# Optimization experiments

Hardware: AMD Instinct MI355X
Metric: run time of the kernel (lower is better)

The kernel has to match this reference:

```python
import jax, jax.numpy as jnp
import numpy as np

LN_EPS = 1e-5

def layernorm(x, w, b):
    mu = jnp.mean(x, axis=-1, keepdims=True)
    var = jnp.mean(jnp.square(x - mu), axis=-1, keepdims=True)
    return (x - mu) * jax.lax.rsqrt(var + LN_EPS) * w + b

def l2_normalize(x, eps=1e-12):
    n = jnp.sqrt(jnp.sum(jnp.square(x), axis=-1, keepdims=True))
    return x / jnp.maximum(n, eps)

def setup_inputs() -> dict:
    key = jax.random.key(0)
    k1, k2 = jax.random.split(key)
    B, D, Npix = 8, 64, 32768
    K, P = 19, 5
    return {
        "base_feature": jax.random.normal(k1, (B, D, Npix), dtype=jnp.float32),
        "means": jax.random.normal(k2, (K, P, D), dtype=jnp.float32) * 0.02,  # trunc_normal_(std=0.02)
        "diagonal": jnp.ones((K, P, D), dtype=jnp.float32),
        "feat_w": jnp.ones((D,), dtype=jnp.float32),
        "feat_b": jnp.zeros((D,), dtype=jnp.float32),
        "mask_w": jnp.ones((K,), dtype=jnp.float32),
        "mask_b": jnp.zeros((K,), dtype=jnp.float32),
    }

def gmm_log_prob(x, mu, scale):
    # x: [N, D]; mu, scale: [KP, D]  (MultivariateNormalDiag with scale_diag=scale)
    # log p = -0.5 * sum(((x-mu)/s)^2) - sum(log s) - 0.5*D*log(2*pi)
    D = x.shape[-1]
    inv2 = 1.0 / jnp.square(scale)                      # [KP, D]
    quad = (jnp.square(x) @ inv2.T                       # [N, KP]
            - 2.0 * (x @ (mu * inv2).T)
            + jnp.sum(jnp.square(mu) * inv2, axis=-1))
    log_norm = jnp.sum(jnp.log(scale), axis=-1) + 0.5 * D * jnp.log(2.0 * jnp.pi)
    return -0.5 * quad - log_norm                        # [N, KP]

def reference(base_feature, means, diagonal, feat_w, feat_b, mask_w, mask_b):
    B, D, Npix = base_feature.shape
    K, P, _ = means.shape
    # 'b c n -> (b n) c'
    _c = jnp.transpose(base_feature, (0, 2, 1)).reshape(B * Npix, D)
    _c = layernorm(_c, feat_w, feat_b)
    _c = l2_normalize(_c)
    means_n = l2_normalize(means)                        # means.data.copy_(l2_normalize(means))
    logp = gmm_log_prob(_c, means_n.reshape(K * P, D), diagonal.reshape(K * P, D))
    final_probs = logp.reshape(-1, K, P)                 # [(b n), K, P]
    _m_prob = jnp.max(final_probs, axis=-1)              # amax over components -> [(b n), K]
    out_seg = layernorm(_m_prob, mask_w, mask_b)         # mask_norm
    # '(b n) k -> b k n'
    out_seg = jnp.transpose(out_seg.reshape(B, Npix, K), (0, 2, 1))
    return out_seg
```

## Files before the change

### kernel.cpp

```cpp
#include <hip/hip_runtime.h>
#include <math.h>

#define BB    8
#define DD    64
#define NPIX  32768
#define KK    19
#define PP    5
#define KP    95
#define KPAD  96

typedef _Float16 half8  __attribute__((ext_vector_type(8)));
typedef __fp16   half2t __attribute__((ext_vector_type(2)));
typedef float    f32x4  __attribute__((ext_vector_type(4)));

union H8 { half8 v; half2t p[4]; };

__global__ __launch_bounds__(64) void gmm_prep(
        const float* __restrict__ means, const float* __restrict__ diag,
        const float* __restrict__ feat_w, const float* __restrict__ feat_b,
        _Float16* __restrict__ Ch, float* __restrict__ cst,
        float* __restrict__ scal) {
    int j = blockIdx.x;
    int d = threadIdx.x;
    if (j < KP) {
        float mu = means[j * DD + d];
        float sc = diag[j * DD + d];
        float ss = mu * mu;
        #pragma unroll
        for (int off = 32; off; off >>= 1) ss += __shfl_xor(ss, off);
        float inv = 1.f / fmaxf(sqrtf(ss), 1e-12f);
        float mn = mu * inv;
        float i2 = 1.f / (sc * sc);
        Ch[j * 128 + 2 * d]     = (_Float16)(mn * i2);
        Ch[j * 128 + 2 * d + 1] = (_Float16)(-0.5f * i2);
        float c1 = mn * mn * i2;
        float c2 = logf(sc);
        #pragma unroll
        for (int off = 32; off; off >>= 1) {
            c1 += __shfl_xor(c1, off);
            c2 += __shfl_xor(c2, off);
        }
        if (d == 0) cst[j] = -0.5f * c1 - c2 - 58.8120661251f;
    } else {
        Ch[95 * 128 + 2 * d]     = (_Float16)0.f;
        Ch[95 * 128 + 2 * d + 1] = (_Float16)0.f;
        float w = feat_w[d], b = feat_b[d];
        float s0 = w * w, s1 = w * b, s2 = b * b;
        #pragma unroll
        for (int off = 32; off; off >>= 1) {
            s0 += __shfl_xor(s0, off);
            s1 += __shfl_xor(s1, off);
            s2 += __shfl_xor(s2, off);
        }
        if (d == 0) { cst[95] = 0.f; scal[0] = s0; scal[1] = s1; scal[2] = s2; }
    }
}

#define LPS 98

__global__ __launch_bounds__(256, 2) void gmm_main(
        const float* __restrict__ bf,
        const float* __restrict__ feat_w, const float* __restrict__ feat_b,
        const float* __restrict__ mask_w, const float* __restrict__ mask_b,
        const _Float16* __restrict__ Ch, const float* __restrict__ cst,
        const float* __restrict__ scal, float* __restrict__ out) {
    __shared__ float lds[4][32 * LPS];

    const int tid  = threadIdx.x;
    const int w    = tid >> 6;
    const int lane = tid & 63;
    const int m15  = lane & 15;
    const int q    = lane >> 4;
    const int bidx = blockIdx.x;
    const int b    = bidx >> 8;
    const int n0   = ((bidx & 255) << 7) + (w << 5);
    float* lp = lds[w];

    const float* xp = bf + (size_t)b * (DD * NPIX) + n0 + m15;
    float xs0[16], xs1[16];
    #pragma unroll
    for (int ks = 0; ks < 4; ++ks)
        #pragma unroll
        for (int i = 0; i < 4; ++i) {
            const size_t off = (size_t)(ks * 16 + q * 4 + i) * NPIX;
            xs0[ks * 4 + i] = xp[off];
            xs1[ks * 4 + i] = xp[off + 16];
        }

    float4 wv[4], bv[4];
    #pragma unroll
    for (int ks = 0; ks < 4; ++ks) {
        wv[ks] = *(const float4*)(feat_w + ks * 16 + q * 4);
        bv[ks] = *(const float4*)(feat_b + ks * 16 + q * 4);
    }

    float S1a = 0.f, S2a = 0.f, S3a = 0.f, S4a = 0.f, S5a = 0.f;
    float S1b = 0.f, S2b = 0.f, S3b = 0.f, S4b = 0.f, S5b = 0.f;
    #pragma unroll
    for (int ks = 0; ks < 4; ++ks)
        #pragma unroll
        for (int i = 0; i < 4; ++i) {
            float wd = ((const float*)&wv[ks])[i];
            float bd = ((const float*)&bv[ks])[i];
            float xa = xs0[ks * 4 + i], xb = xs1[ks * 4 + i];
            float ta = wd * xa, tb = wd * xb;
            S1a += xa; S2a = fmaf(xa, xa, S2a); S3a = fmaf(ta, ta, S3a);
            S4a = fmaf(ta, wd, S4a); S5a = fmaf(ta, bd, S5a);
            S1b += xb; S2b = fmaf(xb, xb, S2b); S3b = fmaf(tb, tb, S3b);
            S4b = fmaf(tb, wd, S4b); S5b = fmaf(tb, bd, S5b);
        }
    S1a += __shfl_xor(S1a, 16); S1a += __shfl_xor(S1a, 32);
    S2a += __shfl_xor(S2a, 16); S2a += __shfl_xor(S2a, 32);
    S3a += __shfl_xor(S3a, 16); S3a += __shfl_xor(S3a, 32);
    S4a += __shfl_xor(S4a, 16); S4a += __shfl_xor(S4a, 32);
    S5a += __shfl_xor(S5a, 16); S5a += __shfl_xor(S5a, 32);
    S1b += __shfl_xor(S1b, 16); S1b += __shfl_xor(S1b, 32);
    S2b += __shfl_xor(S2b, 16); S2b += __shfl_xor(S2b, 32);
    S3b += __shfl_xor(S3b, 16); S3b += __shfl_xor(S3b, 32);
    S4b += __shfl_xor(S4b, 16); S4b += __shfl_xor(S4b, 32);
    S5b += __shfl_xor(S5b, 16); S5b += __shfl_xor(S5b, 32);

    const float W2 = scal[0], WB = scal[1], B2 = scal[2];
    float al0, e0, f0, al1, e1, f1;
    {
        float mu  = S1a * (1.f / 64.f);
        float var = fmaxf(S2a * (1.f / 64.f) - mu * mu, 0.f);
        float r   = rsqrtf(var + 1e-5f);
        float Sy2 = r * r * (S3a - 2.f * mu * S4a + mu * mu * W2)
                  + 2.f * r * (S5a - mu * WB) + B2;
        float invn = 1.f / fmaxf(sqrtf(fmaxf(Sy2, 0.f)), 1e-12f);
        al0 = invn * r; e0 = invn; f0 = -al0 * mu;
    }
    {
        float mu  = S1b * (1.f / 64.f);
        float var = fmaxf(S2b * (1.f / 64.f) - mu * mu, 0.f);
        float r   = rsqrtf(var + 1e-5f);
        float Sy2 = r * r * (S3b - 2.f * mu * S4b + mu * mu * W2)
                  + 2.f * r * (S5b - mu * WB) + B2;
        float invn = 1.f / fmaxf(sqrtf(fmaxf(Sy2, 0.f)), 1e-12f);
        al1 = invn * r; e1 = invn; f1 = -al1 * mu;
    }

    H8 Uh[2][4], Ul[2][4];
    #pragma unroll
    for (int ks = 0; ks < 4; ++ks) {
        #pragma unroll
        for (int i = 0; i < 4; ++i) {
            float wd = ((const float*)&wv[ks])[i];
            float bd = ((const float*)&bv[ks])[i];
            float c0 = fmaf(f0, wd, e0 * bd);
            float c1 = fmaf(f1, wd, e1 * bd);
            float u0 = fmaf(al0, wd * xs0[ks * 4 + i], c0);
            float u1 = fmaf(al1, wd * xs1[ks * 4 + i], c1);
            float q0 = u0 * u0, q1 = u1 * u1;
            half2t h0 = __builtin_amdgcn_cvt_pkrtz(u0, q0);
            half2t h1 = __builtin_amdgcn_cvt_pkrtz(u1, q1);
            half2t l0 = __builtin_amdgcn_cvt_pkrtz(u0 - (float)h0[0], q0 - (float)h0[1]);
            half2t l1 = __builtin_amdgcn_cvt_pkrtz(u1 - (float)h1[0], q1 - (float)h1[1]);
            Uh[0][ks].p[i] = h0; Ul[0][ks].p[i] = l0;
            Uh[1][ks].p[i] = h1; Ul[1][ks].p[i] = l1;
        }
    }

    const _Float16* cb = Ch + (size_t)m15 * 128 + q * 8;
    half8 Ac[4];
    #pragma unroll
    for (int ks = 0; ks < 4; ++ks) Ac[ks] = *(const half8*)(cb + ks * 32);
    float4 cc = *(const float4*)(cst + 4 * q);

    #pragma unroll 2
    for (int t = 0; t < 6; ++t) {
        half8 An[4];
        float4 cn;
        if (t < 5) {
            const _Float16* nb = cb + (size_t)(16 * (t + 1)) * 128;
            #pragma unroll
            for (int ks = 0; ks < 4; ++ks) An[ks] = *(const half8*)(nb + ks * 32);
            cn = *(const float4*)(cst + 16 * (t + 1) + 4 * q);
        }
        f32x4 a0 = {0.f, 0.f, 0.f, 0.f}, a1 = a0;
        #pragma unroll
        for (int ks = 0; ks < 4; ++ks) {
            a0 = __builtin_amdgcn_mfma_f32_16x16x32_f16(Ac[ks], Uh[0][ks].v, a0, 0, 0, 0);
            a1 = __builtin_amdgcn_mfma_f32_16x16x32_f16(Ac[ks], Uh[1][ks].v, a1, 0, 0, 0);
        }
        #pragma unroll
        for (int ks = 0; ks < 4; ++ks) {
            a0 = __builtin_amdgcn_mfma_f32_16x16x32_f16(Ac[ks], Ul[0][ks].v, a0, 0, 0, 0);
            a1 = __builtin_amdgcn_mfma_f32_16x16x32_f16(Ac[ks], Ul[1][ks].v, a1, 0, 0, 0);
        }
        {
            const int j0 = 16 * t + 4 * q;
            float2 v00 = make_float2(a0[0] + cc[0], a0[1] + cc[1]);
            float2 v01 = make_float2(a0[2] + cc[2], a0[3] + cc[3]);
            float2 v10 = make_float2(a1[0] + cc[0], a1[1] + cc[1]);
            float2 v11 = make_float2(a1[2] + cc[2], a1[3] + cc[3]);
            *(float2*)(lp + m15 * LPS + j0)            = v00;
            *(float2*)(lp + m15 * LPS + j0 + 2)        = v01;
            *(float2*)(lp + (16 + m15) * LPS + j0)     = v10;
            *(float2*)(lp + (16 + m15) * LPS + j0 + 2) = v11;
        }
        if (t < 5) {
            #pragma unroll
            for (int ks = 0; ks < 4; ++ks) Ac[ks] = An[ks];
            cc = cn;
        }
    }

    const int px2 = lane & 31;
    const int h   = lane >> 5;
    const int kb  = h ? 9 : 0;
    const int ke  = h ? 19 : 9;
    const float* rowp = lp + px2 * LPS;
    float mv[10];
    float S = 0.f;
    #pragma unroll
    for (int kk = 0; kk < 10; ++kk) {
        const int k = kb + kk;
        float best = -3.4e38f;
        if (k < ke) {
            #pragma unroll
            for (int p = 0; p < PP; ++p)
                best = fmaxf(best, rowp[5 * k + p]);
            S += best;
        }
        mv[kk] = best;
    }
    S += __shfl_xor(S, 32);
    const float mum = S * (1.f / 19.f);
    float V = 0.f;
    #pragma unroll
    for (int kk = 0; kk < 10; ++kk) {
        if (kb + kk < ke) { float t = mv[kk] - mum; V = fmaf(t, t, V); }
    }
    V += __shfl_xor(V, 32);
    const float rm = rsqrtf(V * (1.f / 19.f) + 1e-5f);

    float* op = out + (size_t)b * (KK * NPIX) + n0 + px2;
    #pragma unroll
    for (int kk = 0; kk < 10; ++kk) {
        const int k = kb + kk;
        if (k < ke)
            op[(size_t)k * NPIX] = (mv[kk] - mum) * rm * mask_w[k] + mask_b[k];
    }
}

extern "C" void kernel_launch(void* const* d_in, const int* in_sizes, int n_in,
                              void* d_out, int out_size, void* d_ws, size_t ws_size,
                              hipStream_t stream) {
    const float* base_feature = (const float*)d_in[0];
    const float* means        = (const float*)d_in[1];
    const float* diagonal     = (const float*)d_in[2];
    const float* feat_w       = (const float*)d_in[3];
    const float* feat_b       = (const float*)d_in[4];
    const float* mask_w       = (const float*)d_in[5];
    const float* mask_b       = (const float*)d_in[6];
    float* out = (float*)d_out;

    _Float16* Ch = (_Float16*)d_ws;
    float* cst   = (float*)(Ch + KPAD * 128);
    float* scal  = cst + KPAD;

    gmm_prep<<<KPAD, 64, 0, stream>>>(means, diagonal, feat_w, feat_b, Ch, cst, scal);

    gmm_main<<<(BB * NPIX) / 128, 256, 0, stream>>>(
        base_feature, feat_w, feat_b, mask_w, mask_b, Ch, cst, scal, out);
}
```

Baseline: 138.2 us.

## Pad components to 8 per class so max-over-P reduces in registers without LDS

Each class's 5 mixture components are padded to 8 rows, with the padded rows given a very negative constant, so every 16-row MFMA tile covers exactly two classes. The max over components is then taken directly on the accumulator registers with one cross-lane shuffle, and the mask layernorm runs from registers. This drops the LDS staging buffer and its store/reload round trip. In exchange the MFMA work grows from 6 to 10 tiles per wave, about two thirds more matrix math.

```diff
diff --git a/kernel.cpp b/kernel.cpp
--- a/kernel.cpp
+++ b/kernel.cpp
@@ -7,7 +7,7 @@
 #define KK    19
 #define PP    5
 #define KP    95
-#define KPAD  96
+#define NR    160
 
 typedef _Float16 half8  __attribute__((ext_vector_type(8)));
 typedef __fp16   half2t __attribute__((ext_vector_type(2)));
@@ -18,11 +18,13 @@
 __global__ __launch_bounds__(64) void gmm_prep(
         const float* __restrict__ means, const float* __restrict__ diag,
         const float* __restrict__ feat_w, const float* __restrict__ feat_b,
-        _Float16* __restrict__ Ch, float* __restrict__ cst,
+        _Float16* __restrict__ Cp, float* __restrict__ cstp,
         float* __restrict__ scal) {
-    int j = blockIdx.x;
+    int r = blockIdx.x;
     int d = threadIdx.x;
-    if (j < KP) {
+    int k = r >> 3, p = r & 7;
+    if (k < KK && p < PP) {
+        int j = 5 * k + p;
         float mu = means[j * DD + d];
         float sc = diag[j * DD + d];
         float ss = mu * mu;
@@ -31,8 +33,8 @@
         float inv = 1.f / fmaxf(sqrtf(ss), 1e-12f);
         float mn = mu * inv;
         float i2 = 1.f / (sc * sc);
-        Ch[j * 128 + 2 * d]     = (_Float16)(mn * i2);
-        Ch[j * 128 + 2 * d + 1] = (_Float16)(-0.5f * i2);
+        Cp[r * 128 + 2 * d]     = (_Float16)(mn * i2);
+        Cp[r * 128 + 2 * d + 1] = (_Float16)(-0.5f * i2);
         float c1 = mn * mn * i2;
         float c2 = logf(sc);
         #pragma unroll
@@ -40,32 +42,31 @@
             c1 += __shfl_xor(c1, off);
             c2 += __shfl_xor(c2, off);
         }
-        if (d == 0) cst[j] = -0.5f * c1 - c2 - 58.8120661251f;
+        if (d == 0) cstp[r] = -0.5f * c1 - c2 - 58.8120661251f;
     } else {
-        Ch[95 * 128 + 2 * d]     = (_Float16)0.f;
-        Ch[95 * 128 + 2 * d + 1] = (_Float16)0.f;
-        float w = feat_w[d], b = feat_b[d];
-        float s0 = w * w, s1 = w * b, s2 = b * b;
-        #pragma unroll
-        for (int off = 32; off; off >>= 1) {
-            s0 += __shfl_xor(s0, off);
-            s1 += __shfl_xor(s1, off);
-            s2 += __shfl_xor(s2, off);
-        }
-        if (d == 0) { cst[95] = 0.f; scal[0] = s0; scal[1] = s1; scal[2] = s2; }
+        Cp[r * 128 + 2 * d]     = (_Float16)0.f;
+        Cp[r * 128 + 2 * d + 1] = (_Float16)0.f;
+        if (d == 0) cstp[r] = -3.0e38f;
+        if (r == NR - 1) {
+            float w = feat_w[d], b = feat_b[d];
+            float s0 = w * w, s1 = w * b, s2 = b * b;
+            #pragma unroll
+            for (int off = 32; off; off >>= 1) {
+                s0 += __shfl_xor(s0, off);
+                s1 += __shfl_xor(s1, off);
+                s2 += __shfl_xor(s2, off);
+            }
+            if (d == 0) { scal[0] = s0; scal[1] = s1; scal[2] = s2; }
+        }
     }
 }
-
-#define LPS 98
 
 __global__ __launch_bounds__(256, 2) void gmm_main(
         const float* __restrict__ bf,
         const float* __restrict__ feat_w, const float* __restrict__ feat_b,
         const float* __restrict__ mask_w, const float* __restrict__ mask_b,
-        const _Float16* __restrict__ Ch, const float* __restrict__ cst,
+        const _Float16* __restrict__ Cp, const float* __restrict__ cstp,
         const float* __restrict__ scal, float* __restrict__ out) {
-    __shared__ float lds[4][32 * LPS];
-
     const int tid  = threadIdx.x;
     const int w    = tid >> 6;
     const int lane = tid & 63;
@@ -74,7 +75,6 @@
     const int bidx = blockIdx.x;
     const int b    = bidx >> 8;
     const int n0   = ((bidx & 255) << 7) + (w << 5);
-    float* lp = lds[w];
 
     const float* xp = bf + (size_t)b * (DD * NPIX) + n0 + m15;
     float xs0[16], xs1[16];
@@ -162,21 +162,22 @@
         }
     }
 
-    const _Float16* cb = Ch + (size_t)m15 * 128 + q * 8;
+    float mv0[10], mv1[10];
+    const _Float16* cb = Cp + (size_t)m15 * 128 + q * 8;
     half8 Ac[4];
     #pragma unroll
     for (int ks = 0; ks < 4; ++ks) Ac[ks] = *(const half8*)(cb + ks * 32);
-    float4 cc = *(const float4*)(cst + 4 * q);
+    float4 cc = *(const float4*)(cstp + 4 * q);
 
     #pragma unroll 2
-    for (int t = 0; t < 6; ++t) {
+    for (int t = 0; t < 10; ++t) {
         half8 An[4];
         float4 cn;
-        if (t < 5) {
+        if (t < 9) {
             const _Float16* nb = cb + (size_t)(16 * (t + 1)) * 128;
             #pragma unroll
             for (int ks = 0; ks < 4; ++ks) An[ks] = *(const half8*)(nb + ks * 32);
-            cn = *(const float4*)(cst + 16 * (t + 1) + 4 * q);
+            cn = *(const float4*)(cstp + 16 * (t + 1) + 4 * q);
         }
         f32x4 a0 = {0.f, 0.f, 0.f, 0.f}, a1 = a0;
         #pragma unroll
@@ -189,59 +190,55 @@
             a0 = __builtin_amdgcn_mfma_f32_16x16x32_f16(Ac[ks], Ul[0][ks].v, a0, 0, 0, 0);
             a1 = __builtin_amdgcn_mfma_f32_16x16x32_f16(Ac[ks], Ul[1][ks].v, a1, 0, 0, 0);
         }
-        {
-            const int j0 = 16 * t + 4 * q;
-            float2 v00 = make_float2(a0[0] + cc[0], a0[1] + cc[1]);
-            float2 v01 = make_float2(a0[2] + cc[2], a0[3] + cc[3]);
-            float2 v10 = make_float2(a1[0] + cc[0], a1[1] + cc[1]);
-            float2 v11 = make_float2(a1[2] + cc[2], a1[3] + cc[3]);
-            *(float2*)(lp + m15 * LPS + j0)            = v00;
-            *(float2*)(lp + m15 * LPS + j0 + 2)        = v01;
-            *(float2*)(lp + (16 + m15) * LPS + j0)     = v10;
-            *(float2*)(lp + (16 + m15) * LPS + j0 + 2) = v11;
-        }
-        if (t < 5) {
+        float c0 = fmaxf(fmaxf(a0[0] + cc[0], a0[1] + cc[1]),
+                         fmaxf(a0[2] + cc[2], a0[3] + cc[3]));
+        float c1 = fmaxf(fmaxf(a1[0] + cc[0], a1[1] + cc[1]),
+                         fmaxf(a1[2] + cc[2], a1[3] + cc[3]));
+        c0 = fmaxf(c0, __shfl_xor(c0, 16));
+        c1 = fmaxf(c1, __shfl_xor(c1, 16));
+        mv0[t] = c0;
+        mv1[t] = c1;
+        if (t < 9) {
             #pragma unroll
             for (int ks = 0; ks < 4; ++ks) Ac[ks] = An[ks];
             cc = cn;
         }
     }
 
-    const int px2 = lane & 31;
-    const int h   = lane >> 5;
-    const int kb  = h ? 9 : 0;
-    const int ke  = h ? 19 : 9;
-    const float* rowp = lp + px2 * LPS;
-    float mv[10];
-    float S = 0.f;
-    #pragma unroll
-    for (int kk = 0; kk < 10; ++kk) {
-        const int k = kb + kk;
-        float best = -3.4e38f;
-        if (k < ke) {
-            #pragma unroll
-            for (int p = 0; p < PP; ++p)
-                best = fmaxf(best, rowp[5 * k + p]);
-            S += best;
-        }
-        mv[kk] = best;
-    }
-    S += __shfl_xor(S, 32);
-    const float mum = S * (1.f / 19.f);
-    float V = 0.f;
-    #pragma unroll
-    for (int kk = 0; kk < 10; ++kk) {
-        if (kb + kk < ke) { float t = mv[kk] - mum; V = fmaf(t, t, V); }
-    }
-    V += __shfl_xor(V, 32);
-    const float rm = rsqrtf(V * (1.f / 19.f) + 1e-5f);
-
-    float* op = out + (size_t)b * (KK * NPIX) + n0 + px2;
-    #pragma unroll
-    for (int kk = 0; kk < 10; ++kk) {
-        const int k = kb + kk;
-        if (k < ke)
-            op[(size_t)k * NPIX] = (mv[kk] - mum) * rm * mask_w[k] + mask_b[k];
+    const int qh = (lane >> 5) & 1;
+    float S0 = 0.f, S1 = 0.f;
+    #pragma unroll
+    for (int t = 0; t < 10; ++t) {
+        if (2 * t + qh < KK) { S0 += mv0[t]; S1 += mv1[t]; }
+    }
+    S0 += __shfl_xor(S0, 32);
+    S1 += __shfl_xor(S1, 32);
+    const float mum0 = S0 * (1.f / 19.f);
+    const float mum1 = S1 * (1.f / 19.f);
+    float V0 = 0.f, V1 = 0.f;
+    #pragma unroll
+    for (int t = 0; t < 10; ++t) {
+        if (2 * t + qh < KK) {
+            float d0 = mv0[t] - mum0; V0 = fmaf(d0, d0, V0);
+            float d1 = mv1[t] - mum1; V1 = fmaf(d1, d1, V1);
+        }
+    }
+    V0 += __shfl_xor(V0, 32);
+    V1 += __shfl_xor(V1, 32);
+    const float rm0 = rsqrtf(V0 * (1.f / 19.f) + 1e-5f);
+    const float rm1 = rsqrtf(V1 * (1.f / 19.f) + 1e-5f);
+
+    const int ht   = q & 1;
+    const float mum = ht ? mum1 : mum0;
+    const float rm  = ht ? rm1  : rm0;
+    float* op = out + (size_t)b * (KK * NPIX) + n0 + ht * 16 + m15;
+    #pragma unroll
+    for (int t = 0; t < 10; ++t) {
+        const int k = 2 * t + qh;
+        if (k < KK) {
+            float v = ht ? mv1[t] : mv0[t];
+            op[(size_t)k * NPIX] = (v - mum) * rm * mask_w[k] + mask_b[k];
+        }
     }
 }
 
@@ -257,12 +254,12 @@
     const float* mask_b       = (const float*)d_in[6];
     float* out = (float*)d_out;
 
-    _Float16* Ch = (_Float16*)d_ws;
-    float* cst   = (float*)(Ch + KPAD * 128);
-    float* scal  = cst + KPAD;
-
-    gmm_prep<<<KPAD, 64, 0, stream>>>(means, diagonal, feat_w, feat_b, Ch, cst, scal);
+    _Float16* Cp = (_Float16*)d_ws;
+    float* cstp  = (float*)(Cp + NR * 128);
+    float* scal  = cstp + NR;
+
+    gmm_prep<<<NR, 64, 0, stream>>>(means, diagonal, feat_w, feat_b, Cp, cstp, scal);
 
     gmm_main<<<(BB * NPIX) / 128, 256, 0, stream>>>(
-        base_feature, feat_w, feat_b, mask_w, mask_b, Ch, cst, scal, out);
+        base_feature, feat_w, feat_b, mask_w, mask_b, Cp, cstp, scal, out);
 }
```

Result: slower. 165.3 us (+19.6%).
